# Kernel tuning notes

Measured on AMD Instinct MI355X. Metric: run time of the kernel, lower is better.

## Reference

```python
import jax, jax.numpy as jnp
import numpy as np

B, S, H = 2, 2048, 2048
N = 16               # num heads
NOPE, ROPE, V = 128, 64, 128
QHD = NOPE + ROPE    # 192 per-head q/k dim
QL, KVL = 1536, 512  # q_lora_rank, kv_lora_rank
THETA = 10000.0
SCALE = QHD ** -0.5
EPS = 1e-6


def rmsnorm(x, w):
    var = jnp.mean(x.astype(jnp.float32) ** 2, axis=-1, keepdims=True)
    return (x.astype(jnp.float32) * jax.lax.rsqrt(var + EPS)).astype(x.dtype) * w


def rotate_half(x):
    d = x.shape[-1] // 2
    return jnp.concatenate([-x[..., d:], x[..., :d]], axis=-1)


def setup_inputs() -> dict:
    key = jax.random.key(0)
    ks = jax.random.split(key, 8)
    w = lambda k, shape: jax.random.normal(k, shape, jnp.float32) * 0.02
    return {
        "hidden_states": jax.random.normal(ks[0], (B, S, H), jnp.float32),
        "position_ids": (jnp.arange(B * S, dtype=jnp.int64) % 4096).reshape(B, S),
        "q_a_w": w(ks[1], (QL, H)),
        "q_a_ln_w": jnp.ones((QL,), jnp.float32),
        "q_b_w": w(ks[2], (N * QHD, QL)),
        "kv_a_w": w(ks[3], (KVL + ROPE, H)),
        "kv_a_ln_w": jnp.ones((KVL,), jnp.float32),
        "kv_b_w": w(ks[4], (N * (NOPE + V), KVL)),
        "o_w": w(ks[5], (H, N * V)),
    }


def mla_forward(hidden_states, position_ids, q_a_w, q_a_ln_w, q_b_w,
                kv_a_w, kv_a_ln_w, kv_b_w, o_w):
    b, s, _ = hidden_states.shape
    # ---- Q low-rank path: q_b(rmsnorm(q_a(x))) ----
    q = rmsnorm(hidden_states @ q_a_w.T, q_a_ln_w) @ q_b_w.T
    q = q.reshape(b, s, N, QHD)
    q_nope, q_pe = q[..., :NOPE], q[..., NOPE:]
    # ---- compressed KV + shared rope key ----
    kv_a = hidden_states @ kv_a_w.T                       # [b,s,KVL+ROPE]
    compressed_kv = rmsnorm(kv_a[..., :KVL], kv_a_ln_w)   # [b,s,KVL]
    k_pe = kv_a[..., KVL:].reshape(b, s, 1, ROPE)         # MQA rope key
    # ---- RoPE (default, theta=1e4) from position_ids ----
    inv_freq = 1.0 / (THETA ** (jnp.arange(0, ROPE, 2, dtype=jnp.float32) / ROPE))
    freqs = position_ids.astype(jnp.float32)[..., None] * inv_freq  # [b,s,ROPE/2]
    emb = jnp.concatenate([freqs, freqs], axis=-1)                  # [b,s,ROPE]
    cos = jnp.cos(emb)[:, :, None, :].astype(hidden_states.dtype)   # [b,s,1,ROPE]
    sin = jnp.sin(emb)[:, :, None, :].astype(hidden_states.dtype)
    q_pe = q_pe * cos + rotate_half(q_pe) * sin
    k_pe = k_pe * cos + rotate_half(k_pe) * sin
    # ---- decompress latent KV via kv_b_proj ----
    kv = (compressed_kv @ kv_b_w.T).reshape(b, s, N, NOPE + V)
    k_nope, v = kv[..., :NOPE], kv[..., NOPE:]
    k = jnp.concatenate([k_nope, jnp.broadcast_to(k_pe, (b, s, N, ROPE))], axis=-1)
    qf = jnp.concatenate([q_nope, q_pe], axis=-1)          # [b,s,N,QHD]
    # ---- causal SDPA in bsnd layout ----
    scores = jnp.einsum('bqnd,bknd->bnqk', qf, k) * SCALE  # [b,N,s,s]
    causal = jnp.tril(jnp.ones((s, s), bool))
    scores = jnp.where(causal, scores, jnp.finfo(scores.dtype).min)
    probs = jax.nn.softmax(scores, axis=-1)
    attn = jnp.einsum('bnqk,bknd->bqnd', probs, v)         # [b,s,N,V]
    out = attn.reshape(b, s, N * V) @ o_w.T
    return out


def reference(hidden_states, position_ids, q_a_w, q_a_ln_w, q_b_w,
              kv_a_w, kv_a_ln_w, kv_b_w, o_w):
    return mla_forward(hidden_states, position_ids, q_a_w, q_a_ln_w, q_b_w,
                       kv_a_w, kv_a_ln_w, kv_b_w, o_w)
```

## Files before the change

### kernel.cpp

```cpp
#include <hip/hip_runtime.h>
#include <cstdio>

typedef unsigned short u16;
typedef u16 u16x4 __attribute__((ext_vector_type(4)));
typedef u16 u16x8 __attribute__((ext_vector_type(8)));
typedef __bf16 bf16x8 __attribute__((ext_vector_type(8)));
typedef float f32x4 __attribute__((ext_vector_type(4)));

#define AS1 __attribute__((address_space(1)))
#define AS3 __attribute__((address_space(3)))

#define GLOAD16(gsrc, ldst) __builtin_amdgcn_global_load_lds( \
    (const AS1 void*)(gsrc), (AS3 void*)(ldst), 16, 0, 0)

__device__ __forceinline__ u16 f2bf(float f) {
  unsigned u = __builtin_bit_cast(unsigned, f);
  u += 0x7fffu + ((u >> 16) & 1u);
  return (u16)(u >> 16);
}
__device__ __forceinline__ float bf2f(u16 h) {
  return __builtin_bit_cast(float, (unsigned)h << 16);
}

__global__ __launch_bounds__(256) void cvt_pad_k(const float* __restrict__ src,
                                                 u16* __restrict__ dst,
                                                 long srcN, long dstN) {
  long i = ((long)blockIdx.x * 256 + threadIdx.x) * 8;
  const long stride = (long)gridDim.x * 256 * 8;
  for (; i < dstN; i += stride) {
    u16x8 o = {0,0,0,0,0,0,0,0};
    if (i < srcN) {
      const float4* p = (const float4*)(src + i);
      float4 a = p[0], b = p[1];
      o[0]=f2bf(a.x); o[1]=f2bf(a.y); o[2]=f2bf(a.z); o[3]=f2bf(a.w);
      o[4]=f2bf(b.x); o[5]=f2bf(b.y); o[6]=f2bf(b.z); o[7]=f2bf(b.w);
    }
    *(u16x8*)(dst + i) = o;
  }
}

__global__ __launch_bounds__(256) void rms_k(const u16* __restrict__ src, u16* __restrict__ dst,
                                             const float* __restrict__ w,
                                             int sstride, int dstride, int cols) {
  const int row = blockIdx.x;
  const int tid = threadIdx.x;
  const int nch = cols >> 3;
  float x[8];
  float ss = 0.f;
  if (tid < nch) {
    u16x8 v = *(const u16x8*)(src + (size_t)row * sstride + tid * 8);
#pragma unroll
    for (int j = 0; j < 8; ++j) { x[j] = bf2f(v[j]); ss += x[j] * x[j]; }
  } else {
#pragma unroll
    for (int j = 0; j < 8; ++j) x[j] = 0.f;
  }
#pragma unroll
  for (int off = 1; off < 64; off <<= 1) ss += __shfl_xor(ss, off);
  __shared__ float red[4];
  const int wv = tid >> 6, ln = tid & 63;
  if (ln == 0) red[wv] = ss;
  __syncthreads();
  const float tot = red[0] + red[1] + red[2] + red[3];
  const float rs = 1.0f / sqrtf(tot / (float)cols + 1e-6f);
  if (tid < nch) {
    u16x8 o;
#pragma unroll
    for (int j = 0; j < 8; ++j) o[j] = f2bf(x[j] * rs * w[tid * 8 + j]);
    *(u16x8*)(dst + (size_t)row * dstride + tid * 8) = o;
  }
}

__global__ __launch_bounds__(256) void rope_k(u16* __restrict__ q, const u16* __restrict__ kva,
                                              u16* __restrict__ kpe, const int* __restrict__ pos) {
  const int tok = blockIdx.x;
  const int j = threadIdx.x & 63;
  const int w = threadIdx.x >> 6;
  const float p = (float)pos[tok];
  const int jj = j & 31;
  const float inv = __powf(10000.0f, -(float)jj * (1.0f / 32.0f));
  float s, c;
  __sincosf(p * inv, &s, &c);
  const float sgn = (j < 32) ? -1.0f : 1.0f;
  const int partner = (j < 32) ? j + 32 : j - 32;
  if (w == 0) {
    const float x  = bf2f(kva[(size_t)tok * 640 + 512 + j]);
    const float xp = bf2f(kva[(size_t)tok * 640 + 512 + partner]);
    kpe[(size_t)tok * 64 + j] = f2bf(x * c + sgn * xp * s);
  }
#pragma unroll
  for (int hh = 0; hh < 4; ++hh) {
    const int h = w * 4 + hh;
    const size_t base = (size_t)tok * 3072 + h * 192 + 128;
    const float x  = bf2f(q[base + j]);
    const float xp = bf2f(q[base + partner]);
    q[base + j] = f2bf(x * c + sgn * xp * s);
  }
}

__global__ __launch_bounds__(256) void gemm_bt(const u16* __restrict__ A, const u16* __restrict__ B,
                                               u16* __restrict__ Cb, float* __restrict__ Cf,
                                               int M, int N, int K) {
  __shared__ __attribute__((aligned(16))) u16 As[128 * 64];
  __shared__ __attribute__((aligned(16))) u16 Bs[128 * 64];
  const int tid = threadIdx.x;
  const int m0 = blockIdx.y * 128, n0 = blockIdx.x * 128;
  const int w = tid >> 6, lane = tid & 63;
  const int wr = w >> 1, wc = w & 1;
  const int lr = lane & 15, g = lane >> 4;

  f32x4 acc[4][4] = {};

  for (int k0 = 0; k0 < K; k0 += 64) {
#pragma unroll
    for (int i = 0; i < 4; ++i) {
      const int c = i * 256 + tid;
      const int row = c >> 3, col = (c & 7) << 3;
      GLOAD16(A + (size_t)(m0 + row) * K + k0 + col, &As[c * 8]);
    }
#pragma unroll
    for (int i = 0; i < 4; ++i) {
      const int c = i * 256 + tid;
      const int row = c >> 3, col = (c & 7) << 3;
      GLOAD16(B + (size_t)(n0 + row) * K + k0 + col, &Bs[c * 8]);
    }
    __syncthreads();
    bf16x8 af[4][2], bfr[4][2];
#pragma unroll
    for (int x = 0; x < 4; ++x)
#pragma unroll
      for (int kk = 0; kk < 2; ++kk) {
        af[x][kk]  = *(const bf16x8*)(&As[(wr * 64 + x * 16 + lr) * 64 + kk * 32 + g * 8]);
        bfr[x][kk] = *(const bf16x8*)(&Bs[(wc * 64 + x * 16 + lr) * 64 + kk * 32 + g * 8]);
      }
#pragma unroll
    for (int mi = 0; mi < 4; ++mi)
#pragma unroll
      for (int ni = 0; ni < 4; ++ni)
#pragma unroll
        for (int kk = 0; kk < 2; ++kk)
          acc[mi][ni] = __builtin_amdgcn_mfma_f32_16x16x32_bf16(af[mi][kk], bfr[ni][kk],
                                                                acc[mi][ni], 0, 0, 0);
    __syncthreads();
  }

  const int rb = m0 + wr * 64, cb = n0 + wc * 64;
#pragma unroll
  for (int mi = 0; mi < 4; ++mi)
#pragma unroll
    for (int ni = 0; ni < 4; ++ni)
#pragma unroll
      for (int i = 0; i < 4; ++i) {
        const int r = rb + mi * 16 + g * 4 + i;
        const int cI = cb + ni * 16 + lr;
        if (Cf) Cf[(size_t)r * N + cI] = acc[mi][ni][i];
        else    Cb[(size_t)r * N + cI] = f2bf(acc[mi][ni][i]);
      }
}

__global__ __launch_bounds__(256) void attn_k(const u16* __restrict__ q, const u16* __restrict__ kvb,
                                              const u16* __restrict__ kpe, u16* __restrict__ ao) {
  __shared__ __attribute__((aligned(16))) u16 Ks[64 * 192];
  __shared__ __attribute__((aligned(16))) u16 Vt[128 * 64];

  const float SCALE = 0.07216878364870323f;
  const int bh = blockIdx.x;
  const int b = bh >> 4, h = bh & 15;
  const int j = 15 - blockIdx.y;
  const int tid = threadIdx.x, w = tid >> 6, lane = tid & 63;
  const int lr = lane & 15, g = lane >> 4;

  const int q0 = j * 128;
  const int qrb = q0 + w * 32;
  u16* Psw = &Ks[w * 2304];

  bf16x8 qf[2][6];
#pragma unroll
  for (int m = 0; m < 2; ++m)
#pragma unroll
    for (int kd = 0; kd < 6; ++kd)
      qf[m][kd] = *(const bf16x8*)(q + (size_t)(b * 2048 + qrb + m * 16 + lr) * 3072 +
                                   h * 192 + kd * 32 + g * 8);

  float mrow[2][4], lrow[2][4];
  f32x4 o[2][8] = {};
#pragma unroll
  for (int m = 0; m < 2; ++m)
#pragma unroll
    for (int i = 0; i < 4; ++i) { mrow[m][i] = -1e30f; lrow[m][i] = 0.f; }

  const int nt = (q0 >> 6) + 2;
  for (int t = 0; t < nt; ++t) {
    const int k0 = t * 64;
#pragma unroll
    for (int i = 0; i < 6; ++i) {
      const int c = i * 256 + tid;
      const int row = c / 24, cl = c - row * 24;
      const int cg = cl ^ (row & 7);
      const u16* src = (cg < 16)
        ? (kvb + (size_t)(b * 2048 + k0 + row) * 4096 + h * 256 + cg * 8)
        : (kpe + (size_t)(b * 2048 + k0 + row) * 64 + (cg - 16) * 8);
      GLOAD16(src, &Ks[c * 8]);
    }
    {
      const int kq = tid >> 4;
      const int vc = (tid & 15) << 3;
      u16x8 vv[4];
#pragma unroll
      for (int r = 0; r < 4; ++r)
        vv[r] = *(const u16x8*)(kvb + (size_t)(b * 2048 + k0 + kq * 4 + r) * 4096 + h * 256 + 128 + vc);
#pragma unroll
      for (int e = 0; e < 8; ++e) {
        const int v = vc + e;
        const int cx = (kq >> 1) ^ (v & 7) ^ ((v >> 3) & 7);
        u16x4 tq = {vv[0][e], vv[1][e], vv[2][e], vv[3][e]};
        *(u16x4*)(&Vt[v * 64 + cx * 8 + (kq & 1) * 4]) = tq;
      }
    }
    __syncthreads();

    const bool active = (k0 <= qrb + 31);
    f32x4 sAcc[2][4] = {};
    if (active) {
#pragma unroll
      for (int nf = 0; nf < 4; ++nf) {
        const int rr = nf * 16 + lr;
#pragma unroll
        for (int kd = 0; kd < 6; ++kd) {
          const int ch = (kd * 4 + g) ^ (rr & 7);
          const bf16x8 kf = *(const bf16x8*)(&Ks[rr * 192 + ch * 8]);
#pragma unroll
          for (int m = 0; m < 2; ++m)
            sAcc[m][nf] = __builtin_amdgcn_mfma_f32_16x16x32_bf16(qf[m][kd], kf, sAcc[m][nf], 0, 0, 0);
        }
      }
    }
    __syncthreads();

    if (active) {
#pragma unroll
      for (int m = 0; m < 2; ++m) {
        float sv[4][4];
#pragma unroll
        for (int nf = 0; nf < 4; ++nf)
#pragma unroll
          for (int i = 0; i < 4; ++i) {
            const int qrow = qrb + m * 16 + g * 4 + i;
            const int kcol = k0 + nf * 16 + lr;
            const float vS = sAcc[m][nf][i] * SCALE;
            sv[nf][i] = (kcol > qrow) ? -1e30f : vS;
          }
        float fac[4], mn[4];
#pragma unroll
        for (int i = 0; i < 4; ++i) {
          float rm = fmaxf(fmaxf(sv[0][i], sv[1][i]), fmaxf(sv[2][i], sv[3][i]));
          rm = fmaxf(rm, __shfl_xor(rm, 1));
          rm = fmaxf(rm, __shfl_xor(rm, 2));
          rm = fmaxf(rm, __shfl_xor(rm, 4));
          rm = fmaxf(rm, __shfl_xor(rm, 8));
          mn[i] = fmaxf(mrow[m][i], rm);
          fac[i] = __expf(mrow[m][i] - mn[i]);
          mrow[m][i] = mn[i];
        }
#pragma unroll
        for (int i = 0; i < 4; ++i) {
          float rsum = 0.f;
#pragma unroll
          for (int nf = 0; nf < 4; ++nf) { sv[nf][i] = __expf(sv[nf][i] - mn[i]); rsum += sv[nf][i]; }
          rsum += __shfl_xor(rsum, 1);
          rsum += __shfl_xor(rsum, 2);
          rsum += __shfl_xor(rsum, 4);
          rsum += __shfl_xor(rsum, 8);
          lrow[m][i] = lrow[m][i] * fac[i] + rsum;
        }
#pragma unroll
        for (int nv = 0; nv < 8; ++nv)
#pragma unroll
          for (int i = 0; i < 4; ++i) o[m][nv][i] *= fac[i];
#pragma unroll
        for (int nf = 0; nf < 4; ++nf)
#pragma unroll
          for (int i = 0; i < 4; ++i)
            Psw[(m * 16 + g * 4 + i) * 72 + nf * 16 + lr] = f2bf(sv[nf][i]);
      }
      asm volatile("s_waitcnt lgkmcnt(0)" ::: "memory");

#pragma unroll
      for (int kc = 0; kc < 2; ++kc) {
        bf16x8 vfr[8];
#pragma unroll
        for (int nv = 0; nv < 8; ++nv) {
          const int v = nv * 16 + lr;
          const int cx = (kc * 4 + g) ^ (v & 7) ^ ((v >> 3) & 7);
          vfr[nv] = *(const bf16x8*)(&Vt[v * 64 + cx * 8]);
        }
#pragma unroll
        for (int m = 0; m < 2; ++m) {
          const bf16x8 pf = *(const bf16x8*)(&Psw[(m * 16 + lr) * 72 + kc * 32 + g * 8]);
#pragma unroll
          for (int nv = 0; nv < 8; ++nv)
            o[m][nv] = __builtin_amdgcn_mfma_f32_16x16x32_bf16(pf, vfr[nv], o[m][nv], 0, 0, 0);
        }
      }
    }
    __syncthreads();
  }

#pragma unroll
  for (int m = 0; m < 2; ++m)
#pragma unroll
    for (int i = 0; i < 4; ++i) {
      const float inv = 1.0f / lrow[m][i];
      const size_t tokOff = (size_t)(b * 2048 + qrb + m * 16 + g * 4 + i) * 2048 + h * 128;
#pragma unroll
      for (int nv = 0; nv < 8; ++nv)
        ao[tokOff + nv * 16 + lr] = f2bf(o[m][nv][i] * inv);
    }
}

extern "C" void kernel_launch(void* const* d_in, const int* in_sizes, int n_in,
                              void* d_out, int out_size, void* d_ws, size_t ws_size,
                              hipStream_t stream) {
  const float* hidden  = (const float*)d_in[0];
  const int*   pos     = (const int*)d_in[1];
  const float* q_a_w   = (const float*)d_in[2];
  const float* q_a_ln  = (const float*)d_in[3];
  const float* q_b_w   = (const float*)d_in[4];
  const float* kv_a_w  = (const float*)d_in[5];
  const float* kv_a_ln = (const float*)d_in[6];
  const float* kv_b_w  = (const float*)d_in[7];
  const float* o_w     = (const float*)d_in[8];
  float* out = (float*)d_out;

  char* ws = (char*)d_ws;
  u16* hb  = (u16*)(ws + 0L);
  u16* w1  = (u16*)(ws + 16777216L);
  u16* w2  = (u16*)(ws + 23068672L);
  u16* w3  = (u16*)(ws + 32505856L);
  u16* w4  = (u16*)(ws + 35127296L);
  u16* w5  = (u16*)(ws + 39321600L);
  u16* qa  = (u16*)(ws + 47710208L);
  u16* qb  = (u16*)(ws + 60293120L);
  u16* kva = (u16*)(ws + 85458944L);
  u16* ckv = (u16*)(ws + 90701824L);
  u16* kpe = (u16*)(ws + 94896128L);
  u16* kvb = (u16*)(ws + 95420416L);
  u16* ao  = (u16*)(ws + 128974848L);
  if (ws_size < 145752064UL) { fprintf(stderr, "ws too small: %zu\n", ws_size); return; }

  auto cvt = [&](const float* s, u16* d, long sn, long dn) {
    long blocks = (dn / 8 + 255) / 256; if (blocks > 2048) blocks = 2048;
    cvt_pad_k<<<dim3((unsigned)blocks), dim3(256), 0, stream>>>(s, d, sn, dn);
  };
  cvt(hidden, hb, 4096L * 2048, 4096L * 2048);
  cvt(q_a_w,  w1, 1536L * 2048, 1536L * 2048);
  cvt(q_b_w,  w2, 3072L * 1536, 3072L * 1536);
  cvt(kv_a_w, w3, 576L * 2048,  640L * 2048);
  cvt(kv_b_w, w4, 4096L * 512,  4096L * 512);
  cvt(o_w,    w5, 2048L * 2048, 2048L * 2048);

  gemm_bt<<<dim3(12, 32), 256, 0, stream>>>(hb, w1, qa, nullptr, 4096, 1536, 2048);
  rms_k<<<4096, 256, 0, stream>>>(qa, qa, q_a_ln, 1536, 1536, 1536);
  gemm_bt<<<dim3(24, 32), 256, 0, stream>>>(qa, w2, qb, nullptr, 4096, 3072, 1536);
  gemm_bt<<<dim3(5, 32), 256, 0, stream>>>(hb, w3, kva, nullptr, 4096, 640, 2048);
  rms_k<<<4096, 256, 0, stream>>>(kva, ckv, kv_a_ln, 640, 512, 512);
  rope_k<<<4096, 256, 0, stream>>>(qb, kva, kpe, pos);
  gemm_bt<<<dim3(32, 32), 256, 0, stream>>>(ckv, w4, kvb, nullptr, 4096, 4096, 512);
  attn_k<<<dim3(32, 16), 256, 0, stream>>>(qb, kvb, kpe, ao);
  gemm_bt<<<dim3(16, 32), 256, 0, stream>>>(ao, w5, nullptr, out, 4096, 2048, 2048);
}
```

Before: 474.1 us.

## Double-buffer attention KV tiles with 32-key steps and prefetch overlap

Shrinks the attention K/V tile from 64 to 32 keys and double-buffers the K and transposed V tiles in LDS. The next tile's loads are issued before the current tile's QK and PV MFMAs, and the V transpose write is placed between them, leaving one barrier per tile. This is meant to hide global-load latency and cut LDS use so more blocks can be resident. The P scratch moves to its own buffer with a 36-element row stride, which is not 16-byte aligned for 128-bit LDS reads. The smaller tile also means more loop iterations and barriers overall, and the last step reloads a tile redundantly.

```diff
diff --git a/kernel.cpp b/kernel.cpp
--- a/kernel.cpp
+++ b/kernel.cpp
@@ -160,8 +160,9 @@
 
 __global__ __launch_bounds__(256) void attn_k(const u16* __restrict__ q, const u16* __restrict__ kvb,
                                               const u16* __restrict__ kpe, u16* __restrict__ ao) {
-  __shared__ __attribute__((aligned(16))) u16 Ks[64 * 192];
-  __shared__ __attribute__((aligned(16))) u16 Vt[128 * 64];
+  __shared__ __attribute__((aligned(16))) u16 Ks[2][32 * 192];
+  __shared__ __attribute__((aligned(16))) u16 Vt[2][128 * 32];
+  __shared__ __attribute__((aligned(16))) u16 Ps[4][32 * 36];
 
   const float SCALE = 0.07216878364870323f;
   const int bh = blockIdx.x;
@@ -172,7 +173,7 @@
 
   const int q0 = j * 128;
   const int qrb = q0 + w * 32;
-  u16* Psw = &Ks[w * 2304];
+  u16* Psw = &Ps[w][0];
 
   bf16x8 qf[2][6];
 #pragma unroll
@@ -189,121 +190,152 @@
 #pragma unroll
     for (int i = 0; i < 4; ++i) { mrow[m][i] = -1e30f; lrow[m][i] = 0.f; }
 
-  const int nt = (q0 >> 6) + 2;
-  for (int t = 0; t < nt; ++t) {
-    const int k0 = t * 64;
-#pragma unroll
-    for (int i = 0; i < 6; ++i) {
+  auto stageK = [&](int buf, int tS) {
+    const int k0s = tS * 32;
+#pragma unroll
+    for (int i = 0; i < 3; ++i) {
       const int c = i * 256 + tid;
       const int row = c / 24, cl = c - row * 24;
       const int cg = cl ^ (row & 7);
       const u16* src = (cg < 16)
-        ? (kvb + (size_t)(b * 2048 + k0 + row) * 4096 + h * 256 + cg * 8)
-        : (kpe + (size_t)(b * 2048 + k0 + row) * 64 + (cg - 16) * 8);
-      GLOAD16(src, &Ks[c * 8]);
-    }
-    {
+        ? (kvb + (size_t)(b * 2048 + k0s + row) * 4096 + h * 256 + cg * 8)
+        : (kpe + (size_t)(b * 2048 + k0s + row) * 64 + (cg - 16) * 8);
+      GLOAD16(src, &Ks[buf][c * 8]);
+    }
+  };
+  auto vload = [&](int tS, u16x8 vv[4]) {
+    if (tid < 128) {
       const int kq = tid >> 4;
       const int vc = (tid & 15) << 3;
-      u16x8 vv[4];
 #pragma unroll
       for (int r = 0; r < 4; ++r)
-        vv[r] = *(const u16x8*)(kvb + (size_t)(b * 2048 + k0 + kq * 4 + r) * 4096 + h * 256 + 128 + vc);
+        vv[r] = *(const u16x8*)(kvb + (size_t)(b * 2048 + tS * 32 + kq * 4 + r) * 4096 +
+                                h * 256 + 128 + vc);
+    }
+  };
+  auto vwrite = [&](int buf, const u16x8 vv[4]) {
+    if (tid < 128) {
+      const int kq = tid >> 4;
+      const int vc = (tid & 15) << 3;
 #pragma unroll
       for (int e = 0; e < 8; ++e) {
         const int v = vc + e;
-        const int cx = (kq >> 1) ^ (v & 7) ^ ((v >> 3) & 7);
+        const int cx = (kq >> 1) ^ (v & 3);
         u16x4 tq = {vv[0][e], vv[1][e], vv[2][e], vv[3][e]};
-        *(u16x4*)(&Vt[v * 64 + cx * 8 + (kq & 1) * 4]) = tq;
-      }
-    }
-    __syncthreads();
-
-    const bool active = (k0 <= qrb + 31);
-    f32x4 sAcc[2][4] = {};
-    if (active) {
-#pragma unroll
-      for (int nf = 0; nf < 4; ++nf) {
-        const int rr = nf * 16 + lr;
-#pragma unroll
-        for (int kd = 0; kd < 6; ++kd) {
-          const int ch = (kd * 4 + g) ^ (rr & 7);
-          const bf16x8 kf = *(const bf16x8*)(&Ks[rr * 192 + ch * 8]);
-#pragma unroll
-          for (int m = 0; m < 2; ++m)
-            sAcc[m][nf] = __builtin_amdgcn_mfma_f32_16x16x32_bf16(qf[m][kd], kf, sAcc[m][nf], 0, 0, 0);
+        *(u16x4*)(&Vt[buf][v * 32 + cx * 8 + (kq & 1) * 4]) = tq;
+      }
+    }
+  };
+  auto qk = [&](int cur, f32x4 sAcc[2][2]) {
+#pragma unroll
+    for (int nf = 0; nf < 2; ++nf) {
+      const int rr = nf * 16 + lr;
+#pragma unroll
+      for (int kd = 0; kd < 6; ++kd) {
+        const int ch = (kd * 4 + g) ^ (rr & 7);
+        const bf16x8 kf = *(const bf16x8*)(&Ks[cur][rr * 192 + ch * 8]);
+#pragma unroll
+        for (int m = 0; m < 2; ++m)
+          sAcc[m][nf] = __builtin_amdgcn_mfma_f32_16x16x32_bf16(qf[m][kd], kf, sAcc[m][nf], 0, 0, 0);
+      }
+    }
+  };
+  auto smpv = [&](int cur, int t, f32x4 sAcc[2][2]) {
+    const int k0 = t * 32;
+#pragma unroll
+    for (int m = 0; m < 2; ++m) {
+      float sv[2][4];
+#pragma unroll
+      for (int nf = 0; nf < 2; ++nf)
+#pragma unroll
+        for (int i = 0; i < 4; ++i) {
+          const int qrow = qrb + m * 16 + g * 4 + i;
+          const int kcol = k0 + nf * 16 + lr;
+          const float vS = sAcc[m][nf][i] * SCALE;
+          sv[nf][i] = (kcol > qrow) ? -1e30f : vS;
         }
-      }
-    }
-    __syncthreads();
-
-    if (active) {
-#pragma unroll
-      for (int m = 0; m < 2; ++m) {
-        float sv[4][4];
-#pragma unroll
-        for (int nf = 0; nf < 4; ++nf)
-#pragma unroll
-          for (int i = 0; i < 4; ++i) {
-            const int qrow = qrb + m * 16 + g * 4 + i;
-            const int kcol = k0 + nf * 16 + lr;
-            const float vS = sAcc[m][nf][i] * SCALE;
-            sv[nf][i] = (kcol > qrow) ? -1e30f : vS;
-          }
-        float fac[4], mn[4];
-#pragma unroll
-        for (int i = 0; i < 4; ++i) {
-          float rm = fmaxf(fmaxf(sv[0][i], sv[1][i]), fmaxf(sv[2][i], sv[3][i]));
-          rm = fmaxf(rm, __shfl_xor(rm, 1));
-          rm = fmaxf(rm, __shfl_xor(rm, 2));
-          rm = fmaxf(rm, __shfl_xor(rm, 4));
-          rm = fmaxf(rm, __shfl_xor(rm, 8));
-          mn[i] = fmaxf(mrow[m][i], rm);
-          fac[i] = __expf(mrow[m][i] - mn[i]);
-          mrow[m][i] = mn[i];
-        }
-#pragma unroll
-        for (int i = 0; i < 4; ++i) {
-          float rsum = 0.f;
-#pragma unroll
-          for (int nf = 0; nf < 4; ++nf) { sv[nf][i] = __expf(sv[nf][i] - mn[i]); rsum += sv[nf][i]; }
-          rsum += __shfl_xor(rsum, 1);
-          rsum += __shfl_xor(rsum, 2);
-          rsum += __shfl_xor(rsum, 4);
-          rsum += __shfl_xor(rsum, 8);
-          lrow[m][i] = lrow[m][i] * fac[i] + rsum;
-        }
-#pragma unroll
-        for (int nv = 0; nv < 8; ++nv)
-#pragma unroll
-          for (int i = 0; i < 4; ++i) o[m][nv][i] *= fac[i];
-#pragma unroll
-        for (int nf = 0; nf < 4; ++nf)
-#pragma unroll
-          for (int i = 0; i < 4; ++i)
-            Psw[(m * 16 + g * 4 + i) * 72 + nf * 16 + lr] = f2bf(sv[nf][i]);
-      }
-      asm volatile("s_waitcnt lgkmcnt(0)" ::: "memory");
-
-#pragma unroll
-      for (int kc = 0; kc < 2; ++kc) {
-        bf16x8 vfr[8];
-#pragma unroll
-        for (int nv = 0; nv < 8; ++nv) {
-          const int v = nv * 16 + lr;
-          const int cx = (kc * 4 + g) ^ (v & 7) ^ ((v >> 3) & 7);
-          vfr[nv] = *(const bf16x8*)(&Vt[v * 64 + cx * 8]);
-        }
-#pragma unroll
-        for (int m = 0; m < 2; ++m) {
-          const bf16x8 pf = *(const bf16x8*)(&Psw[(m * 16 + lr) * 72 + kc * 32 + g * 8]);
-#pragma unroll
-          for (int nv = 0; nv < 8; ++nv)
-            o[m][nv] = __builtin_amdgcn_mfma_f32_16x16x32_bf16(pf, vfr[nv], o[m][nv], 0, 0, 0);
-        }
-      }
-    }
-    __syncthreads();
+      float fac[4], mn[4];
+#pragma unroll
+      for (int i = 0; i < 4; ++i) {
+        float rm = fmaxf(sv[0][i], sv[1][i]);
+        rm = fmaxf(rm, __shfl_xor(rm, 1));
+        rm = fmaxf(rm, __shfl_xor(rm, 2));
+        rm = fmaxf(rm, __shfl_xor(rm, 4));
+        rm = fmaxf(rm, __shfl_xor(rm, 8));
+        mn[i] = fmaxf(mrow[m][i], rm);
+        fac[i] = __expf(mrow[m][i] - mn[i]);
+        mrow[m][i] = mn[i];
+      }
+#pragma unroll
+      for (int i = 0; i < 4; ++i) {
+        float rsum = 0.f;
+#pragma unroll
+        for (int nf = 0; nf < 2; ++nf) { sv[nf][i] = __expf(sv[nf][i] - mn[i]); rsum += sv[nf][i]; }
+        rsum += __shfl_xor(rsum, 1);
+        rsum += __shfl_xor(rsum, 2);
+        rsum += __shfl_xor(rsum, 4);
+        rsum += __shfl_xor(rsum, 8);
+        lrow[m][i] = lrow[m][i] * fac[i] + rsum;
+      }
+#pragma unroll
+      for (int nv = 0; nv < 8; ++nv)
+#pragma unroll
+        for (int i = 0; i < 4; ++i) o[m][nv][i] *= fac[i];
+#pragma unroll
+      for (int nf = 0; nf < 2; ++nf)
+#pragma unroll
+        for (int i = 0; i < 4; ++i)
+          Psw[(m * 16 + g * 4 + i) * 36 + nf * 16 + lr] = f2bf(sv[nf][i]);
+    }
+    asm volatile("s_waitcnt lgkmcnt(0)" ::: "memory");
+
+    bf16x8 vfr[8];
+#pragma unroll
+    for (int nv = 0; nv < 8; ++nv) {
+      const int v = nv * 16 + lr;
+      const int cx = g ^ (v & 3);
+      vfr[nv] = *(const bf16x8*)(&Vt[cur][v * 32 + cx * 8]);
+    }
+#pragma unroll
+    for (int m = 0; m < 2; ++m) {
+      const bf16x8 pf = *(const bf16x8*)(&Psw[(m * 16 + lr) * 36 + g * 8]);
+#pragma unroll
+      for (int nv = 0; nv < 8; ++nv)
+        o[m][nv] = __builtin_amdgcn_mfma_f32_16x16x32_bf16(pf, vfr[nv], o[m][nv], 0, 0, 0);
+    }
+  };
+
+  const int nt = (q0 >> 5) + 4;
+  {
+    u16x8 vv[4];
+    vload(0, vv);
+    stageK(0, 0);
+    vwrite(0, vv);
+  }
+  for (int t = 0; t < nt; t += 2) {
+    {
+      __syncthreads();
+      u16x8 vn[4];
+      vload(t + 1, vn);
+      stageK(1, t + 1);
+      const bool active = (t * 32 <= qrb + 31);
+      f32x4 sAcc[2][2] = {};
+      if (active) qk(0, sAcc);
+      vwrite(1, vn);
+      if (active) smpv(0, t, sAcc);
+    }
+    {
+      __syncthreads();
+      const int ts = (t + 2 < nt) ? t + 2 : nt - 1;
+      u16x8 vn[4];
+      vload(ts, vn);
+      stageK(0, ts);
+      const bool active = ((t + 1) * 32 <= qrb + 31);
+      f32x4 sAcc[2][2] = {};
+      if (active) qk(1, sAcc);
+      vwrite(0, vn);
+      if (active) smpv(1, t + 1, sAcc);
+    }
   }
 
 #pragma unroll
```

New measurement: 545.2 us. 1.15x slower.

## Double-buffer K tiles and prefetch V in attention kernel

Applied to the files above, without the earlier changes.

The attention kernel now holds two K shared-memory buffers. Each iteration issues the global-to-LDS loads for the next K/rope tile and the register loads for the next V tile before running the QK MFMAs on the current tile, so memory latency overlaps with compute. The V transpose into LDS is moved to the end of each iteration, after a barrier. The per-thread load addresses are precomputed once, and explicit waitcnt and barrier intrinsics replace __syncthreads. In exchange, LDS use per block grows to about 64KB, which may reduce occupancy.

```diff
diff --git a/kernel.cpp b/kernel.cpp
--- a/kernel.cpp
+++ b/kernel.cpp
@@ -160,7 +160,7 @@
 
 __global__ __launch_bounds__(256) void attn_k(const u16* __restrict__ q, const u16* __restrict__ kvb,
                                               const u16* __restrict__ kpe, u16* __restrict__ ao) {
-  __shared__ __attribute__((aligned(16))) u16 Ks[64 * 192];
+  __shared__ __attribute__((aligned(16))) u16 Ks[2][64 * 192];
   __shared__ __attribute__((aligned(16))) u16 Vt[128 * 64];
 
   const float SCALE = 0.07216878364870323f;
@@ -172,7 +172,6 @@
 
   const int q0 = j * 128;
   const int qrb = q0 + w * 32;
-  u16* Psw = &Ks[w * 2304];
 
   bf16x8 qf[2][6];
 #pragma unroll
@@ -182,6 +181,30 @@
       qf[m][kd] = *(const bf16x8*)(q + (size_t)(b * 2048 + qrb + m * 16 + lr) * 3072 +
                                    h * 192 + kd * 32 + g * 8);
 
+  const u16* kbase[6];
+  int kstep[6], klds[6];
+#pragma unroll
+  for (int i = 0; i < 6; ++i) {
+    const int c = i * 256 + tid;
+    const int row = c / 24, cl = c - row * 24;
+    const int cg = cl ^ (row & 7);
+    klds[i] = c * 8;
+    if (cg < 16) { kbase[i] = kvb + (size_t)(b * 2048 + row) * 4096 + h * 256 + cg * 8;
+                   kstep[i] = 64 * 4096; }
+    else         { kbase[i] = kpe + (size_t)(b * 2048 + row) * 64 + (cg - 16) * 8;
+                   kstep[i] = 64 * 64; }
+  }
+  const int kq = tid >> 4, vc = (tid & 15) << 3;
+  const u16* vbase = kvb + (size_t)(b * 2048 + kq * 4) * 4096 + h * 256 + 128 + vc;
+  int vlds[8];
+#pragma unroll
+  for (int e = 0; e < 8; ++e) {
+    const int v = vc + e;
+    const int cx = (kq >> 1) ^ (v & 7) ^ ((v >> 3) & 7);
+    vlds[e] = v * 64 + cx * 8 + (kq & 1) * 4;
+  }
+  u16x8 vreg[4];
+
   float mrow[2][4], lrow[2][4];
   f32x4 o[2][8] = {};
 #pragma unroll
@@ -190,36 +213,34 @@
     for (int i = 0; i < 4; ++i) { mrow[m][i] = -1e30f; lrow[m][i] = 0.f; }
 
   const int nt = (q0 >> 6) + 2;
+
+#pragma unroll
+  for (int r = 0; r < 4; ++r) vreg[r] = *(const u16x8*)(vbase + (size_t)r * 4096);
+#pragma unroll
+  for (int i = 0; i < 6; ++i) GLOAD16(kbase[i], &Ks[0][klds[i]]);
+  asm volatile("s_waitcnt vmcnt(0)" ::: "memory");
+  __builtin_amdgcn_s_barrier();
+  __builtin_amdgcn_sched_barrier(0);
+#pragma unroll
+  for (int e = 0; e < 8; ++e) {
+    u16x4 tq = {vreg[0][e], vreg[1][e], vreg[2][e], vreg[3][e]};
+    *(u16x4*)(&Vt[vlds[e]]) = tq;
+  }
+
   for (int t = 0; t < nt; ++t) {
-    const int k0 = t * 64;
-#pragma unroll
-    for (int i = 0; i < 6; ++i) {
-      const int c = i * 256 + tid;
-      const int row = c / 24, cl = c - row * 24;
-      const int cg = cl ^ (row & 7);
-      const u16* src = (cg < 16)
-        ? (kvb + (size_t)(b * 2048 + k0 + row) * 4096 + h * 256 + cg * 8)
-        : (kpe + (size_t)(b * 2048 + k0 + row) * 64 + (cg - 16) * 8);
-      GLOAD16(src, &Ks[c * 8]);
-    }
-    {
-      const int kq = tid >> 4;
-      const int vc = (tid & 15) << 3;
-      u16x8 vv[4];
-#pragma unroll
-      for (int r = 0; r < 4; ++r)
-        vv[r] = *(const u16x8*)(kvb + (size_t)(b * 2048 + k0 + kq * 4 + r) * 4096 + h * 256 + 128 + vc);
-#pragma unroll
-      for (int e = 0; e < 8; ++e) {
-        const int v = vc + e;
-        const int cx = (kq >> 1) ^ (v & 7) ^ ((v >> 3) & 7);
-        u16x4 tq = {vv[0][e], vv[1][e], vv[2][e], vv[3][e]};
-        *(u16x4*)(&Vt[v * 64 + cx * 8 + (kq & 1) * 4]) = tq;
-      }
-    }
-    __syncthreads();
-
-    const bool active = (k0 <= qrb + 31);
+    const int cur = t & 1;
+    u16* KsC = &Ks[cur][0];
+    u16* Psw = KsC + w * 2304;
+    const int ts = (t + 1 < nt) ? t + 1 : nt - 1;
+
+#pragma unroll
+    for (int i = 0; i < 6; ++i)
+      GLOAD16(kbase[i] + (size_t)ts * kstep[i], &Ks[cur ^ 1][klds[i]]);
+#pragma unroll
+    for (int r = 0; r < 4; ++r)
+      vreg[r] = *(const u16x8*)(vbase + (size_t)ts * 64 * 4096 + (size_t)r * 4096);
+
+    const bool active = (t * 64 <= qrb + 31);
     f32x4 sAcc[2][4] = {};
     if (active) {
 #pragma unroll
@@ -228,16 +249,19 @@
 #pragma unroll
         for (int kd = 0; kd < 6; ++kd) {
           const int ch = (kd * 4 + g) ^ (rr & 7);
-          const bf16x8 kf = *(const bf16x8*)(&Ks[rr * 192 + ch * 8]);
+          const bf16x8 kf = *(const bf16x8*)(&KsC[rr * 192 + ch * 8]);
 #pragma unroll
           for (int m = 0; m < 2; ++m)
             sAcc[m][nf] = __builtin_amdgcn_mfma_f32_16x16x32_bf16(qf[m][kd], kf, sAcc[m][nf], 0, 0, 0);
         }
       }
     }
-    __syncthreads();
+    asm volatile("s_waitcnt lgkmcnt(0)" ::: "memory");
+    __builtin_amdgcn_s_barrier();
+    __builtin_amdgcn_sched_barrier(0);
 
     if (active) {
+      const int k0 = t * 64;
 #pragma unroll
       for (int m = 0; m < 2; ++m) {
         float sv[4][4];
@@ -303,7 +327,14 @@
         }
       }
     }
-    __syncthreads();
+    asm volatile("s_waitcnt vmcnt(0) lgkmcnt(0)" ::: "memory");
+    __builtin_amdgcn_s_barrier();
+    __builtin_amdgcn_sched_barrier(0);
+#pragma unroll
+    for (int e = 0; e < 8; ++e) {
+      u16x4 tq = {vreg[0][e], vreg[1][e], vreg[2][e], vreg[3][e]};
+      *(u16x4*)(&Vt[vlds[e]]) = tq;
+    }
   }
 
 #pragma unroll
```

After: 481.2 us. Within noise of the previous version (+1.5%).

## Process 128-key tiles per iteration in attention, halving barrier count

Applied to the files above, without the earlier changes.

The causal attention loop now stages 128 keys per iteration instead of 64. It loads a double-size K tile and two transposed V sub-tiles, then runs two QK^T blocks and two softmax/PV updates back to back through a shared lambda. The goal is to halve the number of loop iterations and __syncthreads barriers, and to put more independent MFMA work between barriers. In exchange, LDS use roughly doubles per block, which may reduce how many blocks fit on a CU, and it raises register pressure from holding two score accumulators.

```diff
diff --git a/kernel.cpp b/kernel.cpp
--- a/kernel.cpp
+++ b/kernel.cpp
@@ -160,8 +160,8 @@
 
 __global__ __launch_bounds__(256) void attn_k(const u16* __restrict__ q, const u16* __restrict__ kvb,
                                               const u16* __restrict__ kpe, u16* __restrict__ ao) {
-  __shared__ __attribute__((aligned(16))) u16 Ks[64 * 192];
-  __shared__ __attribute__((aligned(16))) u16 Vt[128 * 64];
+  __shared__ __attribute__((aligned(16))) u16 Ks[128 * 192];
+  __shared__ __attribute__((aligned(16))) u16 Vt[2][128 * 64];
 
   const float SCALE = 0.07216878364870323f;
   const int bh = blockIdx.x;
@@ -189,11 +189,78 @@
 #pragma unroll
     for (int i = 0; i < 4; ++i) { mrow[m][i] = -1e30f; lrow[m][i] = 0.f; }
 
-  const int nt = (q0 >> 6) + 2;
+  auto smpv = [&](f32x4 sAcc[2][4], int kbase, const u16* VtH) {
+#pragma unroll
+    for (int m = 0; m < 2; ++m) {
+      float sv[4][4];
+#pragma unroll
+      for (int nf = 0; nf < 4; ++nf)
+#pragma unroll
+        for (int i = 0; i < 4; ++i) {
+          const int qrow = qrb + m * 16 + g * 4 + i;
+          const int kcol = kbase + nf * 16 + lr;
+          const float vS = sAcc[m][nf][i] * SCALE;
+          sv[nf][i] = (kcol > qrow) ? -1e30f : vS;
+        }
+      float fac[4], mn[4];
+#pragma unroll
+      for (int i = 0; i < 4; ++i) {
+        float rm = fmaxf(fmaxf(sv[0][i], sv[1][i]), fmaxf(sv[2][i], sv[3][i]));
+        rm = fmaxf(rm, __shfl_xor(rm, 1));
+        rm = fmaxf(rm, __shfl_xor(rm, 2));
+        rm = fmaxf(rm, __shfl_xor(rm, 4));
+        rm = fmaxf(rm, __shfl_xor(rm, 8));
+        mn[i] = fmaxf(mrow[m][i], rm);
+        fac[i] = __expf(mrow[m][i] - mn[i]);
+        mrow[m][i] = mn[i];
+      }
+#pragma unroll
+      for (int i = 0; i < 4; ++i) {
+        float rsum = 0.f;
+#pragma unroll
+        for (int nf = 0; nf < 4; ++nf) { sv[nf][i] = __expf(sv[nf][i] - mn[i]); rsum += sv[nf][i]; }
+        rsum += __shfl_xor(rsum, 1);
+        rsum += __shfl_xor(rsum, 2);
+        rsum += __shfl_xor(rsum, 4);
+        rsum += __shfl_xor(rsum, 8);
+        lrow[m][i] = lrow[m][i] * fac[i] + rsum;
+      }
+#pragma unroll
+      for (int nv = 0; nv < 8; ++nv)
+#pragma unroll
+        for (int i = 0; i < 4; ++i) o[m][nv][i] *= fac[i];
+#pragma unroll
+      for (int nf = 0; nf < 4; ++nf)
+#pragma unroll
+        for (int i = 0; i < 4; ++i)
+          Psw[(m * 16 + g * 4 + i) * 72 + nf * 16 + lr] = f2bf(sv[nf][i]);
+    }
+    asm volatile("s_waitcnt lgkmcnt(0)" ::: "memory");
+
+#pragma unroll
+    for (int kc = 0; kc < 2; ++kc) {
+      bf16x8 vfr[8];
+#pragma unroll
+      for (int nv = 0; nv < 8; ++nv) {
+        const int v = nv * 16 + lr;
+        const int cx = (kc * 4 + g) ^ (v & 7) ^ ((v >> 3) & 7);
+        vfr[nv] = *(const bf16x8*)(&VtH[v * 64 + cx * 8]);
+      }
+#pragma unroll
+      for (int m = 0; m < 2; ++m) {
+        const bf16x8 pf = *(const bf16x8*)(&Psw[(m * 16 + lr) * 72 + kc * 32 + g * 8]);
+#pragma unroll
+        for (int nv = 0; nv < 8; ++nv)
+          o[m][nv] = __builtin_amdgcn_mfma_f32_16x16x32_bf16(pf, vfr[nv], o[m][nv], 0, 0, 0);
+      }
+    }
+  };
+
+  const int nt = (q0 >> 7) + 1;
   for (int t = 0; t < nt; ++t) {
-    const int k0 = t * 64;
-#pragma unroll
-    for (int i = 0; i < 6; ++i) {
+    const int k0 = t * 128;
+#pragma unroll
+    for (int i = 0; i < 12; ++i) {
       const int c = i * 256 + tid;
       const int row = c / 24, cl = c - row * 24;
       const int cg = cl ^ (row & 7);
@@ -202,26 +269,29 @@
         : (kpe + (size_t)(b * 2048 + k0 + row) * 64 + (cg - 16) * 8);
       GLOAD16(src, &Ks[c * 8]);
     }
-    {
+#pragma unroll
+    for (int hh = 0; hh < 2; ++hh) {
       const int kq = tid >> 4;
       const int vc = (tid & 15) << 3;
       u16x8 vv[4];
 #pragma unroll
       for (int r = 0; r < 4; ++r)
-        vv[r] = *(const u16x8*)(kvb + (size_t)(b * 2048 + k0 + kq * 4 + r) * 4096 + h * 256 + 128 + vc);
+        vv[r] = *(const u16x8*)(kvb + (size_t)(b * 2048 + k0 + hh * 64 + kq * 4 + r) * 4096 +
+                                h * 256 + 128 + vc);
 #pragma unroll
       for (int e = 0; e < 8; ++e) {
         const int v = vc + e;
         const int cx = (kq >> 1) ^ (v & 7) ^ ((v >> 3) & 7);
         u16x4 tq = {vv[0][e], vv[1][e], vv[2][e], vv[3][e]};
-        *(u16x4*)(&Vt[v * 64 + cx * 8 + (kq & 1) * 4]) = tq;
-      }
-    }
-    __syncthreads();
-
-    const bool active = (k0 <= qrb + 31);
-    f32x4 sAcc[2][4] = {};
-    if (active) {
+        *(u16x4*)(&Vt[hh][v * 64 + cx * 8 + (kq & 1) * 4]) = tq;
+      }
+    }
+    __syncthreads();
+
+    const bool actA = (k0 <= qrb + 31);
+    const bool actB = (k0 + 64 <= qrb + 31);
+    f32x4 sA[2][4] = {};
+    if (actA) {
 #pragma unroll
       for (int nf = 0; nf < 4; ++nf) {
         const int rr = nf * 16 + lr;
@@ -231,78 +301,29 @@
           const bf16x8 kf = *(const bf16x8*)(&Ks[rr * 192 + ch * 8]);
 #pragma unroll
           for (int m = 0; m < 2; ++m)
-            sAcc[m][nf] = __builtin_amdgcn_mfma_f32_16x16x32_bf16(qf[m][kd], kf, sAcc[m][nf], 0, 0, 0);
+            sA[m][nf] = __builtin_amdgcn_mfma_f32_16x16x32_bf16(qf[m][kd], kf, sA[m][nf], 0, 0, 0);
         }
       }
     }
     __syncthreads();
 
-    if (active) {
-#pragma unroll
-      for (int m = 0; m < 2; ++m) {
-        float sv[4][4];
-#pragma unroll
-        for (int nf = 0; nf < 4; ++nf)
-#pragma unroll
-          for (int i = 0; i < 4; ++i) {
-            const int qrow = qrb + m * 16 + g * 4 + i;
-            const int kcol = k0 + nf * 16 + lr;
-            const float vS = sAcc[m][nf][i] * SCALE;
-            sv[nf][i] = (kcol > qrow) ? -1e30f : vS;
-          }
-        float fac[4], mn[4];
-#pragma unroll
-        for (int i = 0; i < 4; ++i) {
-          float rm = fmaxf(fmaxf(sv[0][i], sv[1][i]), fmaxf(sv[2][i], sv[3][i]));
-          rm = fmaxf(rm, __shfl_xor(rm, 1));
-          rm = fmaxf(rm, __shfl_xor(rm, 2));
-          rm = fmaxf(rm, __shfl_xor(rm, 4));
-          rm = fmaxf(rm, __shfl_xor(rm, 8));
-          mn[i] = fmaxf(mrow[m][i], rm);
-          fac[i] = __expf(mrow[m][i] - mn[i]);
-          mrow[m][i] = mn[i];
+    f32x4 sB[2][4] = {};
+    if (actB) {
+#pragma unroll
+      for (int nf = 0; nf < 4; ++nf) {
+        const int rr = 64 + nf * 16 + lr;
+#pragma unroll
+        for (int kd = 0; kd < 6; ++kd) {
+          const int ch = (kd * 4 + g) ^ (rr & 7);
+          const bf16x8 kf = *(const bf16x8*)(&Ks[rr * 192 + ch * 8]);
+#pragma unroll
+          for (int m = 0; m < 2; ++m)
+            sB[m][nf] = __builtin_amdgcn_mfma_f32_16x16x32_bf16(qf[m][kd], kf, sB[m][nf], 0, 0, 0);
         }
-#pragma unroll
-        for (int i = 0; i < 4; ++i) {
-          float rsum = 0.f;
-#pragma unroll
-          for (int nf = 0; nf < 4; ++nf) { sv[nf][i] = __expf(sv[nf][i] - mn[i]); rsum += sv[nf][i]; }
-          rsum += __shfl_xor(rsum, 1);
-          rsum += __shfl_xor(rsum, 2);
-          rsum += __shfl_xor(rsum, 4);
-          rsum += __shfl_xor(rsum, 8);
-          lrow[m][i] = lrow[m][i] * fac[i] + rsum;
-        }
-#pragma unroll
-        for (int nv = 0; nv < 8; ++nv)
-#pragma unroll
-          for (int i = 0; i < 4; ++i) o[m][nv][i] *= fac[i];
-#pragma unroll
-        for (int nf = 0; nf < 4; ++nf)
-#pragma unroll
-          for (int i = 0; i < 4; ++i)
-            Psw[(m * 16 + g * 4 + i) * 72 + nf * 16 + lr] = f2bf(sv[nf][i]);
-      }
-      asm volatile("s_waitcnt lgkmcnt(0)" ::: "memory");
-
-#pragma unroll
-      for (int kc = 0; kc < 2; ++kc) {
-        bf16x8 vfr[8];
-#pragma unroll
-        for (int nv = 0; nv < 8; ++nv) {
-          const int v = nv * 16 + lr;
-          const int cx = (kc * 4 + g) ^ (v & 7) ^ ((v >> 3) & 7);
-          vfr[nv] = *(const bf16x8*)(&Vt[v * 64 + cx * 8]);
-        }
-#pragma unroll
-        for (int m = 0; m < 2; ++m) {
-          const bf16x8 pf = *(const bf16x8*)(&Psw[(m * 16 + lr) * 72 + kc * 32 + g * 8]);
-#pragma unroll
-          for (int nv = 0; nv < 8; ++nv)
-            o[m][nv] = __builtin_amdgcn_mfma_f32_16x16x32_bf16(pf, vfr[nv], o[m][nv], 0, 0, 0);
-        }
-      }
-    }
+      }
+    }
+    if (actA) smpv(sA, k0, &Vt[0][0]);
+    if (actB) smpv(sB, k0 + 64, &Vt[1][0]);
     __syncthreads();
   }
 
```

Result: slower. 485.6 us (+2.4%).
